# Performance work log

Measured on AMD Instinct MI355X. Metric: run time of the kernel, lower is better.

## Reference

```python
import jax, jax.numpy as jnp
import numpy as np

QMAX = 127.0

def setup_inputs() -> dict:
    key = jax.random.key(0)
    kx, kw, ks = jax.random.split(key, 3)
    B, S, D_IN, D_OUT = 4, 2048, 4096, 4096
    x = jax.random.normal(kx, (B, S, D_IN), dtype=jnp.float16)
    # int8 weight buffer, same distribution as torch.randint(-127, 127)
    weight = jax.random.randint(kw, (D_OUT, D_IN), -127, 127, dtype=jnp.int32).astype(jnp.int8)
    # per-output-channel weight scales (fp16 buffer); small positive values
    weight_scales = (jax.random.uniform(ks, (D_OUT,), dtype=jnp.float32) * 0.01 + 1e-4).astype(jnp.float16)
    return {"x": x, "weight": weight, "weight_scales": weight_scales}

def reference(x, weight, weight_scales):
    # x: [B, S, D_in] fp16; weight: [D_out, D_in] int8; weight_scales: [D_out] fp16
    x32 = x.astype(jnp.float32)
    # dynamic per-token absmax quantization: scale = absmax / 127
    absmax = jnp.max(jnp.abs(x32), axis=-1, keepdims=True)      # [B, S, 1]
    x_scales = jnp.maximum(absmax / QMAX, 1e-8)
    q = jnp.round(x32 / x_scales)                                # in [-127, 127]
    q = jnp.clip(q, -QMAX, QMAX).astype(jnp.int8)
    # int8 GEMM accumulated in int32 (cupy.matmul on int32 in the original)
    y = jnp.einsum('bsk,nk->bsn', q.astype(jnp.int32), weight.astype(jnp.int32),
                   preferred_element_type=jnp.int32)             # [B, S, D_out]
    # dequant: per-token activation scale * per-channel weight scale
    y = y.astype(jnp.float32) * x_scales * weight_scales.astype(jnp.float32)[None, None, :]
    return y.astype(jnp.float16)
```

## Files before the change

kernel.cpp:

```cpp
#include <hip/hip_runtime.h>
#include <stdint.h>

typedef int int32x4  __attribute__((ext_vector_type(4)));
typedef int int32x16 __attribute__((ext_vector_type(16)));

constexpr int K_DIM = 4096;
constexpr int N_DIM = 4096;
constexpr float QMAXF = 127.0f;

__global__ __launch_bounds__(256) void quant_rows(const float* __restrict__ x,
                                                  int8_t* __restrict__ q,
                                                  float* __restrict__ scales) {
    const int row = blockIdx.x;
    const int tid = threadIdx.x;
    const size_t base = (size_t)row * K_DIM;

    const float4* xv = reinterpret_cast<const float4*>(x + base);
    float4 v[4];
#pragma unroll
    for (int i = 0; i < 4; ++i) v[i] = xv[tid + 256 * i];

    float m = 0.0f;
#pragma unroll
    for (int i = 0; i < 4; ++i)
        m = fmaxf(m, fmaxf(fmaxf(fabsf(v[i].x), fabsf(v[i].y)),
                           fmaxf(fabsf(v[i].z), fabsf(v[i].w))));
#pragma unroll
    for (int off = 32; off > 0; off >>= 1) m = fmaxf(m, __shfl_xor(m, off));

    __shared__ float wmax[4];
    if ((tid & 63) == 0) wmax[tid >> 6] = m;
    __syncthreads();
    const float am = fmaxf(fmaxf(wmax[0], wmax[1]), fmaxf(wmax[2], wmax[3]));
    const float scale = fmaxf(am * (1.0f / 127.0f), 1e-8f);
    if (tid == 0) scales[row] = scale;
    const float inv = 1.0f / scale;

    int* qw = reinterpret_cast<int*>(q + base);
#pragma unroll
    for (int i = 0; i < 4; ++i) {
        float f0 = fminf(QMAXF, fmaxf(-QMAXF, rintf(v[i].x * inv)));
        float f1 = fminf(QMAXF, fmaxf(-QMAXF, rintf(v[i].y * inv)));
        float f2 = fminf(QMAXF, fmaxf(-QMAXF, rintf(v[i].z * inv)));
        float f3 = fminf(QMAXF, fmaxf(-QMAXF, rintf(v[i].w * inv)));
        int b0 = ((int)f0) & 255, b1 = ((int)f1) & 255;
        int b2 = ((int)f2) & 255, b3 = ((int)f3) & 255;
        qw[tid + 256 * i] = b0 | (b1 << 8) | (b2 << 16) | (b3 << 24);
    }
}

__global__ __launch_bounds__(256) void pack_w(const int* __restrict__ w,
                                              int8_t* __restrict__ w8) {
    const int idx = blockIdx.x * 256 + threadIdx.x;
    const int4 v = reinterpret_cast<const int4*>(w)[idx];
    int packed = (v.x & 255) | ((v.y & 255) << 8) | ((v.z & 255) << 16) | ((v.w & 255) << 24);
    reinterpret_cast<int*>(w8)[idx] = packed;
}

constexpr int BM = 256, BN = 256, BKB = 128;
constexpr int NT = K_DIM / BKB;

#define GLL(src, dst)                                                          \
    __builtin_amdgcn_global_load_lds(                                          \
        (const __attribute__((address_space(1))) unsigned int*)(src),          \
        (__attribute__((address_space(3))) unsigned int*)(dst), 16, 0, 0)

#define MFMA32(a, b, c) __builtin_amdgcn_mfma_i32_32x32x32_i8((a), (b), (c), 0, 0, 0)

#define MFMA4(ACC, AF, BF)                                                     \
    {                                                                          \
        __builtin_amdgcn_s_setprio(1);                                         \
        ACC = MFMA32(AF[0], BF[0], ACC);                                       \
        ACC = MFMA32(AF[1], BF[1], ACC);                                       \
        ACC = MFMA32(AF[2], BF[2], ACC);                                       \
        ACC = MFMA32(AF[3], BF[3], ACC);                                       \
        __builtin_amdgcn_s_setprio(0);                                         \
    }

__global__ __launch_bounds__(512, 2) void w8a8_gemm256(
        const int8_t* __restrict__ A, const int8_t* __restrict__ B,
        const float* __restrict__ asc, const float* __restrict__ wsc,
        float* __restrict__ C, int M) {
    extern __shared__ int8_t lds[];

    const int tid  = threadIdx.x;
    const int lane = tid & 63;
    const int wave = tid >> 6;

    const int nwg = gridDim.x;
    const int bid = blockIdx.x;
    const int swz = (bid & 7) * (nwg >> 3) + (bid >> 3);
    const int NB  = N_DIM / BN;
    const int brow = (swz / NB) * BM;
    const int bcol = (swz % NB) * BN;

    const int wm = wave >> 2;
    const int wn = wave & 3;
    const int l31 = lane & 31;
    const int lh  = lane >> 5;

    const int rowin = tid >> 3;
    const int gsl   = ((tid & 7) ^ (rowin & 7)) * 16;
    const int8_t* gA = A + (size_t)(brow + rowin) * K_DIM + gsl;
    const int8_t* gB = B + (size_t)(bcol + rowin) * K_DIM + gsl;
    const size_t chunk_g = (size_t)64 * K_DIM;
    const int segb = wave * 1024;

    const int sb = lh ^ (l31 & 7);
    const int baseA = (wm * 128 + l31) * BKB;
    const int baseB = (wn * 64  + l31) * BKB;

    int32x16 acc[4][2];
#pragma unroll
    for (int i = 0; i < 4; ++i)
#pragma unroll
        for (int j = 0; j < 2; ++j)
#pragma unroll
            for (int e = 0; e < 16; ++e) acc[i][j][e] = 0;

#pragma unroll
    for (int c = 0; c < 4; ++c) {
        GLL(gA + c * chunk_g, lds + c * 8192 + segb);
        GLL(gB + c * chunk_g, lds + 65536 + c * 8192 + segb);
    }
    asm volatile("s_waitcnt vmcnt(0)" ::: "memory");
    __builtin_amdgcn_s_barrier();

    int32x4 af[2][4], bf[2][4];

    for (int t = 0; t < NT; ++t) {
        const int8_t* Ab = lds + (t & 1) * 32768;
        const int8_t* Bb = lds + 65536 + (t & 1) * 32768;
        int8_t* dA = lds + ((t + 1) & 1) * 32768;
        int8_t* dB = lds + 65536 + ((t + 1) & 1) * 32768;
        const bool pf = (t + 1 < NT);
        const size_t kk = (size_t)(t + 1) * BKB;

        __builtin_amdgcn_s_barrier();
        if (pf) {
#pragma unroll
            for (int c = 0; c < 4; ++c)
                GLL(gA + kk + c * chunk_g, dA + c * 8192 + segb);
            asm volatile("s_waitcnt vmcnt(4)" ::: "memory");
        } else {
            asm volatile("s_waitcnt vmcnt(0)" ::: "memory");
        }
        __builtin_amdgcn_s_barrier();

#pragma unroll
        for (int ks = 0; ks < 4; ++ks) {
            af[0][ks] = *(const int32x4*)(Ab + baseA + ((sb ^ (2 * ks)) * 16));
            bf[0][ks] = *(const int32x4*)(Bb + baseB + ((sb ^ (2 * ks)) * 16));
        }

#pragma unroll
        for (int ks = 0; ks < 4; ++ks)
            bf[1][ks] = *(const int32x4*)(Bb + baseB + 4096 + ((sb ^ (2 * ks)) * 16));
        MFMA4(acc[0][0], af[0], bf[0]);

#pragma unroll
        for (int ks = 0; ks < 4; ++ks)
            af[1][ks] = *(const int32x4*)(Ab + baseA + 4096 + ((sb ^ (2 * ks)) * 16));
        MFMA4(acc[0][1], af[0], bf[1]);

#pragma unroll
        for (int ks = 0; ks < 4; ++ks)
            af[0][ks] = *(const int32x4*)(Ab + baseA + 8192 + ((sb ^ (2 * ks)) * 16));
        MFMA4(acc[1][0], af[1], bf[0]);

        MFMA4(acc[1][1], af[1], bf[1]);

#pragma unroll
        for (int ks = 0; ks < 4; ++ks)
            af[1][ks] = *(const int32x4*)(Ab + baseA + 12288 + ((sb ^ (2 * ks)) * 16));
        MFMA4(acc[2][0], af[0], bf[0]);

        if (pf) {
#pragma unroll
            for (int c = 0; c < 4; ++c)
                GLL(gB + kk + c * chunk_g, dB + c * 8192 + segb);
        }
        MFMA4(acc[2][1], af[0], bf[1]);

        MFMA4(acc[3][0], af[1], bf[0]);
        MFMA4(acc[3][1], af[1], bf[1]);
    }

#pragma unroll
    for (int ni = 0; ni < 2; ++ni) {
        const int col = bcol + wn * 64 + ni * 32 + l31;
        const float ws = wsc[col];
#pragma unroll
        for (int mi = 0; mi < 4; ++mi) {
            const int rowb = brow + wm * 128 + mi * 32 + 4 * lh;
#pragma unroll
            for (int r = 0; r < 16; ++r) {
                const int row = rowb + (r & 3) + 8 * (r >> 2);
                float o = (float)acc[mi][ni][r] * asc[row] * ws;
                o = (float)(_Float16)o;
                C[(size_t)row * N_DIM + col] = o;
            }
        }
    }
}

extern "C" void kernel_launch(void* const* d_in, const int* in_sizes, int n_in,
                              void* d_out, int out_size, void* d_ws, size_t ws_size,
                              hipStream_t stream) {
    const float* x   = (const float*)d_in[0];
    const int*   w   = (const int*)d_in[1];
    const float* wsc = (const float*)d_in[2];
    float* out = (float*)d_out;

    const int K = K_DIM;
    const int M = in_sizes[0] / K;
    const int N = N_DIM;

    int8_t* q   = (int8_t*)d_ws;
    int8_t* w8  = (int8_t*)d_ws + (size_t)M * K;
    float*  asc = (float*)((char*)d_ws + (size_t)M * K + (size_t)N * K);

    quant_rows<<<M, 256, 0, stream>>>(x, q, asc);
    pack_w<<<(N * (K / 4)) / 256, 256, 0, stream>>>(w, w8);
    const int grid = (M / BM) * (N / BN);
    w8a8_gemm256<<<grid, 512, 131072, stream>>>(q, w8, asc, wsc, out, M);
}
```

Measured before the change: 197.3 us.

## Split LDS tiles into two 64-byte K halves with new XOR swizzle

Changes the shared-memory layout of the A and B tiles. Each 128-row by 128-byte chunk is now stored as two separate 64-byte K-half planes with a 4-way XOR swizzle, and the global-to-LDS load mapping and fragment read offsets are updated to match. The aim is to cut LDS bank conflicts on the 16-byte fragment reads and to keep global loads coalesced as contiguous 64-byte row segments. The cost is a more intricate address mapping, where any indexing mismatch would silently corrupt results.

```diff
diff --git a/kernel.cpp b/kernel.cpp
--- a/kernel.cpp
+++ b/kernel.cpp
@@ -77,6 +77,12 @@
         __builtin_amdgcn_s_setprio(0);                                         \
     }
 
+#define LDFRAG(DST, P, OFF)                                                    \
+    DST[0] = *(const int32x4*)((P) + (OFF) + sl0b);                            \
+    DST[1] = *(const int32x4*)((P) + (OFF) + (sl0b ^ 32));                     \
+    DST[2] = *(const int32x4*)((P) + (OFF) + 16384 + sl0b);                    \
+    DST[3] = *(const int32x4*)((P) + (OFF) + 16384 + (sl0b ^ 32));
+
 __global__ __launch_bounds__(512, 2) void w8a8_gemm256(
         const int8_t* __restrict__ A, const int8_t* __restrict__ B,
         const float* __restrict__ asc, const float* __restrict__ wsc,
@@ -99,16 +105,16 @@
     const int l31 = lane & 31;
     const int lh  = lane >> 5;
 
-    const int rowin = tid >> 3;
-    const int gsl   = ((tid & 7) ^ (rowin & 7)) * 16;
-    const int8_t* gA = A + (size_t)(brow + rowin) * K_DIM + gsl;
-    const int8_t* gB = B + (size_t)(bcol + rowin) * K_DIM + gsl;
-    const size_t chunk_g = (size_t)64 * K_DIM;
+    const int rowch = wave * 16 + (lane >> 2);
+    const int g     = ((lane & 3) ^ ((lane >> 3) & 3)) * 16;
+    const int8_t* gA = A + (size_t)(brow + rowch) * K_DIM + g;
+    const int8_t* gB = B + (size_t)(bcol + rowch) * K_DIM + g;
     const int segb = wave * 1024;
 
-    const int sb = lh ^ (l31 & 7);
-    const int baseA = (wm * 128 + l31) * BKB;
-    const int baseB = (wn * 64  + l31) * BKB;
+    const int q4   = (l31 >> 1) & 3;
+    const int sl0b = (lh ^ q4) * 16;
+    const int baseA = (wm * 128 + l31) * 64;
+    const int baseB = (wn * 64  + l31) * 64;
 
     int32x16 acc[4][2];
 #pragma unroll
@@ -120,8 +126,9 @@
 
 #pragma unroll
     for (int c = 0; c < 4; ++c) {
-        GLL(gA + c * chunk_g, lds + c * 8192 + segb);
-        GLL(gB + c * chunk_g, lds + 65536 + c * 8192 + segb);
+        const size_t cg = (size_t)(c & 1) * 128 * K_DIM + (c >> 1) * 64;
+        GLL(gA + cg, lds + c * 8192 + segb);
+        GLL(gB + cg, lds + 65536 + c * 8192 + segb);
     }
     asm volatile("s_waitcnt vmcnt(0)" ::: "memory");
     __builtin_amdgcn_s_barrier();
@@ -129,8 +136,8 @@
     int32x4 af[2][4], bf[2][4];
 
     for (int t = 0; t < NT; ++t) {
-        const int8_t* Ab = lds + (t & 1) * 32768;
-        const int8_t* Bb = lds + 65536 + (t & 1) * 32768;
+        const int8_t* Ab = lds + (t & 1) * 32768 + baseA;
+        const int8_t* Bb = lds + 65536 + (t & 1) * 32768 + baseB;
         int8_t* dA = lds + ((t + 1) & 1) * 32768;
         int8_t* dB = lds + 65536 + ((t + 1) & 1) * 32768;
         const bool pf = (t + 1 < NT);
@@ -139,46 +146,39 @@
         __builtin_amdgcn_s_barrier();
         if (pf) {
 #pragma unroll
-            for (int c = 0; c < 4; ++c)
-                GLL(gA + kk + c * chunk_g, dA + c * 8192 + segb);
+            for (int c = 0; c < 4; ++c) {
+                const size_t cg = (size_t)(c & 1) * 128 * K_DIM + (c >> 1) * 64;
+                GLL(gA + kk + cg, dA + c * 8192 + segb);
+            }
             asm volatile("s_waitcnt vmcnt(4)" ::: "memory");
         } else {
             asm volatile("s_waitcnt vmcnt(0)" ::: "memory");
         }
         __builtin_amdgcn_s_barrier();
 
-#pragma unroll
-        for (int ks = 0; ks < 4; ++ks) {
-            af[0][ks] = *(const int32x4*)(Ab + baseA + ((sb ^ (2 * ks)) * 16));
-            bf[0][ks] = *(const int32x4*)(Bb + baseB + ((sb ^ (2 * ks)) * 16));
-        }
-
-#pragma unroll
-        for (int ks = 0; ks < 4; ++ks)
-            bf[1][ks] = *(const int32x4*)(Bb + baseB + 4096 + ((sb ^ (2 * ks)) * 16));
+        LDFRAG(af[0], Ab, 0);
+        LDFRAG(bf[0], Bb, 0);
+
+        LDFRAG(bf[1], Bb, 2048);
         MFMA4(acc[0][0], af[0], bf[0]);
 
-#pragma unroll
-        for (int ks = 0; ks < 4; ++ks)
-            af[1][ks] = *(const int32x4*)(Ab + baseA + 4096 + ((sb ^ (2 * ks)) * 16));
+        LDFRAG(af[1], Ab, 2048);
         MFMA4(acc[0][1], af[0], bf[1]);
 
-#pragma unroll
-        for (int ks = 0; ks < 4; ++ks)
-            af[0][ks] = *(const int32x4*)(Ab + baseA + 8192 + ((sb ^ (2 * ks)) * 16));
+        LDFRAG(af[0], Ab, 4096);
         MFMA4(acc[1][0], af[1], bf[0]);
 
         MFMA4(acc[1][1], af[1], bf[1]);
 
-#pragma unroll
-        for (int ks = 0; ks < 4; ++ks)
-            af[1][ks] = *(const int32x4*)(Ab + baseA + 12288 + ((sb ^ (2 * ks)) * 16));
+        LDFRAG(af[1], Ab, 6144);
         MFMA4(acc[2][0], af[0], bf[0]);
 
         if (pf) {
 #pragma unroll
-            for (int c = 0; c < 4; ++c)
-                GLL(gB + kk + c * chunk_g, dB + c * 8192 + segb);
+            for (int c = 0; c < 4; ++c) {
+                const size_t cg = (size_t)(c & 1) * 128 * K_DIM + (c >> 1) * 64;
+                GLL(gB + kk + cg, dB + c * 8192 + segb);
+            }
         }
         MFMA4(acc[2][1], af[0], bf[1]);
 
```

Measured after the change: 194.2 us. Within noise of the previous version (-1.6%).
